# Kernel tuning notes

Hardware: AMD Instinct MI355X
Metric: run time of the kernel (lower is better)

## Reference

```python
import jax, jax.numpy as jnp
import numpy as np

NEG = -1e9  # additive mask value


def _longformer_attn(x, kv_mask, Wq, bq, Wk, bk, Wv, bv, Wqg, bqg, Wkg, bkg, Wvg, bvg, Wo, bo, H, w, G):
    # x: [B, S, E]; kv_mask: [B, S] (mask*-1 > 0 => global; first G tokens are global by construction)
    B, S, E = x.shape
    D = E // H
    scale = 1.0 / float(D) ** 0.5

    def proj(W, b):  # -> [B, H, S, D]
        return (x @ W + b).reshape(B, S, H, D).transpose(0, 2, 1, 3)

    q = proj(Wq, bq) * scale
    k = proj(Wk, bk)
    v = proj(Wv, bv)

    nc = S // w  # number of query chunks of size w
    # banded keys/values: each chunk of w queries sees a 3w key band (prev/cur/next chunk)
    idx = (jnp.arange(nc) * w)[:, None] + jnp.arange(3 * w)[None, :]  # [nc, 3w] into padded seq

    def band(t):  # [B,H,S,D] -> [B,H,nc,3w,D]
        tp = jnp.pad(t, ((0, 0), (0, 0), (w, w), (0, 0)))
        return tp[:, :, idx, :]

    k3, v3 = band(k), band(v)
    qc = q.reshape(B, H, nc, w, D)
    s_win = jnp.einsum('bhcwd,bhced->bhcwe', qc, k3)  # [B,H,nc,w,3w]

    i = jnp.arange(w)[:, None]
    j = jnp.arange(3 * w)[None, :]
    rel_ok = (j >= i) & (j <= i + 2 * w)  # |key_pos - query_pos| <= w
    keypos = (jnp.arange(nc) * w)[:, None, None] + (jnp.arange(3 * w) - w)[None, None, :]  # [nc,1,3w]
    ok = rel_ok[None] & (keypos >= 0) & (keypos < S) & (keypos >= G)  # global keys handled separately
    s_win = jnp.where(ok[None, None], s_win, NEG)

    # every query also attends to the G global keys (standard projections)
    s_g = jnp.einsum('bhqd,bhgd->bhqg', q, k[:, :, :G])  # [B,H,S,G]
    s_all = jnp.concatenate([s_g, s_win.reshape(B, H, S, 3 * w)], axis=-1)
    p = jax.nn.softmax(s_all, axis=-1)  # joint softmax over global + window keys
    p_g, p_w = p[..., :G], p[..., G:].reshape(B, H, nc, w, 3 * w)

    out = jnp.einsum('bhcwe,bhced->bhcwd', p_w, v3).reshape(B, H, S, D)
    out = out + jnp.einsum('bhqg,bhgd->bhqd', p_g, v[:, :, :G])

    # global query rows: full attention over all tokens with the *global* projections
    qg = (x @ Wqg + bqg).reshape(B, S, H, D).transpose(0, 2, 1, 3)[:, :, :G] * scale
    kg = (x @ Wkg + bkg).reshape(B, S, H, D).transpose(0, 2, 1, 3)
    vg = (x @ Wvg + bvg).reshape(B, S, H, D).transpose(0, 2, 1, 3)
    pg = jax.nn.softmax(jnp.einsum('bhgd,bhsd->bhgs', qg, kg), axis=-1)  # [B,H,G,S]
    out = out.at[:, :, :G].set(jnp.einsum('bhgs,bhsd->bhgd', pg, vg))

    ctx = out.transpose(0, 2, 1, 3).reshape(B, S, E)
    return ctx @ Wo + bo  # wrapper's self.output Linear


def setup_inputs() -> dict:
    key = jax.random.key(0)
    B, S, E, H, w, G = 2, 4096, 1024, 16, 256, 64
    ks = jax.random.split(key, 20)
    x = jax.random.normal(ks[0], (B, S, E), dtype=jnp.float32)
    # key_value_states acts as the mask source: (kv * -1) > 0 marks global tokens
    kv = jnp.zeros((B, S), dtype=jnp.float32).at[:, :G].set(-1.0)

    def lin(k1, k2):
        return (jax.random.normal(k1, (E, E), dtype=jnp.float32) * 0.02,
                jax.random.normal(k2, (E,), dtype=jnp.float32) * 0.02)

    Wq, bq = lin(ks[1], ks[2])
    Wk, bk = lin(ks[3], ks[4])
    Wv, bv = lin(ks[5], ks[6])
    Wqg, bqg = lin(ks[7], ks[8])
    Wkg, bkg = lin(ks[9], ks[10])
    Wvg, bvg = lin(ks[11], ks[12])
    Wo, bo = lin(ks[13], ks[14])
    return {"hidden_states": x, "key_value_states": kv,
            "Wq": Wq, "bq": bq, "Wk": Wk, "bk": bk, "Wv": Wv, "bv": bv,
            "Wqg": Wqg, "bqg": bqg, "Wkg": Wkg, "bkg": bkg, "Wvg": Wvg, "bvg": bvg,
            "Wo": Wo, "bo": bo, "num_heads": H, "window": w, "num_global": G}


def reference(hidden_states, key_value_states, Wq, bq, Wk, bk, Wv, bv, Wqg, bqg, Wkg, bkg, Wvg, bvg, Wo, bo, num_heads, window, num_global):
    return _longformer_attn(hidden_states, key_value_states, Wq, bq, Wk, bk, Wv, bv,
                            Wqg, bqg, Wkg, bkg, Wvg, bvg, Wo, bo,
                            num_heads, window, num_global)
```

## Files before the change

### kernel.cpp

```cpp
#include <hip/hip_runtime.h>

typedef _Float16 half_t;
typedef _Float16 h8 __attribute__((ext_vector_type(8)));
typedef _Float16 h4 __attribute__((ext_vector_type(4)));
typedef float f4 __attribute__((ext_vector_type(4)));

#define DEV __device__ __forceinline__

constexpr int Bc = 2, Sc = 4096, Ec = 1024, Hc = 16, Dc = 64, Wc = 256, Gc = 64;
constexpr float QSCALE = 0.125f;
constexpr float NEGV = -1e9f;

DEV f4 mfma16(h8 a, h8 b, f4 c) {
  return __builtin_amdgcn_mfma_f32_16x16x32_f16(a, b, c, 0, 0, 0);
}

DEV void gl_lds16(const half_t* g, half_t* l) {
  __builtin_amdgcn_global_load_lds((const __attribute__((address_space(1))) void*)g,
                                   (__attribute__((address_space(3))) void*)l, 16, 0, 0);
}


__global__ void cvt_x_kernel(const float* __restrict__ x, half_t* __restrict__ xh) {
  int i = blockIdx.x * 256 + threadIdx.x;
  float4 v = ((const float4*)x)[i];
  h4 o;
  o[0] = (half_t)v.x; o[1] = (half_t)v.y; o[2] = (half_t)v.z; o[3] = (half_t)v.w;
  ((h4*)xh)[i] = o;
}

__global__ void wcvt_kernel(const float* __restrict__ W, half_t* __restrict__ Wt) {
  __shared__ float tile[64][65];
  const int bx = blockIdx.x & 15, by = blockIdx.x >> 4;
  const int tx = threadIdx.x & 63, ty = threadIdx.x >> 6;
  const int n0 = bx * 64, k0 = by * 64;
#pragma unroll
  for (int i = 0; i < 16; ++i) {
    int k = ty + i * 4;
    tile[k][tx] = W[(size_t)(k0 + k) * Ec + n0 + tx];
  }
  __syncthreads();
#pragma unroll
  for (int i = 0; i < 16; ++i) {
    int n = ty + i * 4;
    Wt[(size_t)(n0 + n) * Ec + k0 + tx] = (half_t)tile[tx][n];
  }
}

__global__ __launch_bounds__(256) void gemm_proj(const half_t* __restrict__ A,
                                                 const half_t* __restrict__ Bt,
                                                 const float* __restrict__ bcat,
                                                 half_t* __restrict__ qh, half_t* __restrict__ kh,
                                                 half_t* __restrict__ vt, half_t* __restrict__ kgh,
                                                 half_t* __restrict__ vgt, half_t* __restrict__ qgh) {
  __shared__ __align__(16) half_t Ash[128 * 32];
  __shared__ __align__(16) half_t Bsh[128 * 32];
  const int tid = threadIdx.x;
  const int wv = tid >> 6, lane = tid & 63;
  const int mr = lane & 15, qd = lane >> 4;
  const int wv_m = wv >> 1, wv_n = wv & 1;
  const int col0 = blockIdx.x * 128;
  const int row0 = blockIdx.y * 128;
  const int g = col0 >> 10;

  f4 acc[4][4] = {};

  for (int k0 = 0; k0 < Ec; k0 += 32) {
#pragma unroll
    for (int i = 0; i < 2; ++i) {
      int slot = wv * 128 + i * 64 + lane;
      int r = slot >> 2;
      int kc = (slot & 3) ^ (r & 3);
      gl_lds16(A + (size_t)(row0 + r) * Ec + k0 + kc * 8, Ash + (size_t)(wv * 128 + i * 64) * 8);
      gl_lds16(Bt + (size_t)(col0 + r) * Ec + k0 + kc * 8, Bsh + (size_t)(wv * 128 + i * 64) * 8);
    }
    __syncthreads();
    h8 af[4], bf[4];
#pragma unroll
    for (int mt = 0; mt < 4; ++mt) {
      int r = wv_m * 64 + mt * 16 + mr;
      af[mt] = *(const h8*)(Ash + (size_t)((r << 2) | (qd ^ (r & 3))) * 8);
    }
#pragma unroll
    for (int nt = 0; nt < 4; ++nt) {
      int r = wv_n * 64 + nt * 16 + mr;
      bf[nt] = *(const h8*)(Bsh + (size_t)((r << 2) | (qd ^ (r & 3))) * 8);
    }
#pragma unroll
    for (int mt = 0; mt < 4; ++mt)
#pragma unroll
      for (int nt = 0; nt < 4; ++nt)
        acc[mt][nt] = mfma16(af[mt], bf[nt], acc[mt][nt]);
    __syncthreads();
  }

  const float scale = (g == 0 || g == 5) ? QSCALE : 1.0f;
#pragma unroll
  for (int mt = 0; mt < 4; ++mt) {
#pragma unroll
    for (int nt = 0; nt < 4; ++nt) {
      const int C = col0 + wv_n * 64 + nt * 16 + mr;
      const float bval = bcat[C];
      const int c1 = C & 1023, hh = c1 >> 6, d = c1 & 63;
      const int Rbase = row0 + wv_m * 64 + mt * 16 + qd * 4;
      f4 a = acc[mt][nt];
      if (g == 2 || g == 4) {
        half_t* O = (g == 2) ? vt : vgt;
        int b = Rbase >> 12, s = Rbase & 4095;
        h4 pk;
#pragma unroll
        for (int r = 0; r < 4; ++r) pk[r] = (half_t)(a[r] + bval);
        *(h4*)(O + ((size_t)(b * Hc + hh) * Dc + d) * Sc + s) = pk;
      } else if (g == 5) {
#pragma unroll
        for (int r = 0; r < 4; ++r) {
          int R = Rbase + r;
          int b = R >> 12, s = R & 4095;
          if (s < Gc)
            qgh[((size_t)(b * Hc + hh) * Gc + s) * Dc + d] = (half_t)((a[r] + bval) * scale);
        }
      } else {
        half_t* O = (g == 0) ? qh : (g == 1) ? kh : kgh;
#pragma unroll
        for (int r = 0; r < 4; ++r) {
          int R = Rbase + r;
          int b = R >> 12, s = R & 4095;
          O[((size_t)(b * Hc + hh) * Sc + s) * Dc + d] = (half_t)((a[r] + bval) * scale);
        }
      }
    }
  }
}

__global__ __launch_bounds__(256) void gemm_out(const half_t* __restrict__ A,
                                                const half_t* __restrict__ Bt,
                                                const float* __restrict__ bias,
                                                float* __restrict__ O) {
  __shared__ __align__(16) half_t Ash[128 * 32];
  __shared__ __align__(16) half_t Bsh[128 * 32];
  const int tid = threadIdx.x;
  const int wv = tid >> 6, lane = tid & 63;
  const int mr = lane & 15, qd = lane >> 4;
  const int wv_m = wv >> 1, wv_n = wv & 1;
  const int col0 = blockIdx.x * 128;
  const int row0 = blockIdx.y * 128;

  f4 acc[4][4] = {};

  for (int k0 = 0; k0 < Ec; k0 += 32) {
#pragma unroll
    for (int i = 0; i < 2; ++i) {
      int slot = wv * 128 + i * 64 + lane;
      int r = slot >> 2;
      int kc = (slot & 3) ^ (r & 3);
      gl_lds16(A + (size_t)(row0 + r) * Ec + k0 + kc * 8, Ash + (size_t)(wv * 128 + i * 64) * 8);
      gl_lds16(Bt + (size_t)(col0 + r) * Ec + k0 + kc * 8, Bsh + (size_t)(wv * 128 + i * 64) * 8);
    }
    __syncthreads();
    h8 af[4], bf[4];
#pragma unroll
    for (int mt = 0; mt < 4; ++mt) {
      int r = wv_m * 64 + mt * 16 + mr;
      af[mt] = *(const h8*)(Ash + (size_t)((r << 2) | (qd ^ (r & 3))) * 8);
    }
#pragma unroll
    for (int nt = 0; nt < 4; ++nt) {
      int r = wv_n * 64 + nt * 16 + mr;
      bf[nt] = *(const h8*)(Bsh + (size_t)((r << 2) | (qd ^ (r & 3))) * 8);
    }
#pragma unroll
    for (int mt = 0; mt < 4; ++mt)
#pragma unroll
      for (int nt = 0; nt < 4; ++nt)
        acc[mt][nt] = mfma16(af[mt], bf[nt], acc[mt][nt]);
    __syncthreads();
  }

#pragma unroll
  for (int mt = 0; mt < 4; ++mt) {
#pragma unroll
    for (int nt = 0; nt < 4; ++nt) {
      const int C = col0 + wv_n * 64 + nt * 16 + mr;
      const float bval = bias[C];
      const int Rbase = row0 + wv_m * 64 + mt * 16 + qd * 4;
      f4 a = acc[mt][nt];
#pragma unroll
      for (int r = 0; r < 4; ++r)
        O[(size_t)(Rbase + r) * Ec + C] = a[r] + bval;
    }
  }
}

__global__ __launch_bounds__(256) void win_attn(const half_t* __restrict__ qh,
                                                const half_t* __restrict__ kh,
                                                const half_t* __restrict__ vt,
                                                half_t* __restrict__ ctx) {
  constexpr int PST = 88;
  __shared__ __align__(16) half_t Kb[2][64 * 64];
  __shared__ __align__(16) half_t Vb[2][64 * 64];
  __shared__ __align__(16) half_t Pl[4][16 * PST];
  const int bid = blockIdx.x;
  const int qc = bid & 15, h = (bid >> 4) & 15, b = bid >> 8;
  const int qs = qc << 8;
  const int tid = threadIdx.x, wv = tid >> 6, lane = tid & 63;
  const int mr = lane & 15, qd = lane >> 4;
  const int qw = qs + wv * 64;
  const size_t bh = (size_t)(b * Hc + h);
  const half_t* qb = qh + bh * Sc * Dc;
  const half_t* kb = kh + bh * Sc * Dc;
  const half_t* vb = vt + bh * Dc * Sc;
  half_t* Pw = &Pl[wv][0];

  h8 qf[4][2];
#pragma unroll
  for (int qt = 0; qt < 4; ++qt) {
    const half_t* qrow = qb + (size_t)(qw + qt * 16 + mr) * Dc;
    qf[qt][0] = *(const h8*)(qrow + qd * 8);
    qf[qt][1] = *(const h8*)(qrow + 32 + qd * 8);
  }

  int tiles[14];
  int nT = 0;
  tiles[nT++] = 0;
  {
    int lo = qs - Wc; if (lo < Gc) lo = Gc;
    int hi = qs + 448; if (hi > Sc - 64) hi = Sc - 64;
    for (int kp0 = lo; kp0 <= hi; kp0 += 64) tiles[nT++] = kp0;
  }

  auto stage = [&](int kp0, int bi) {
#pragma unroll
    for (int i = 0; i < 2; ++i) {
      const int seg = wv * 2 + i;
      const int s = seg * 64 + lane;
      const int r = s >> 3;
      const int kc = (s & 7) ^ (r & 7);
      gl_lds16(kb + (size_t)(kp0 + r) * Dc + kc * 8, &Kb[bi][seg * 512]);
      gl_lds16(vb + (size_t)r * Sc + kp0 + kc * 8, &Vb[bi][seg * 512]);
    }
  };

  float m_run[4], l_run[4];
  f4 acc[4][4] = {};
#pragma unroll
  for (int qt = 0; qt < 4; ++qt) { m_run[qt] = -1e30f; l_run[qt] = 0.f; }

  stage(tiles[0], 0);

  for (int t = 0; t < nT; ++t) {
    __syncthreads();
    if (t + 1 < nT) stage(tiles[t + 1], (t + 1) & 1);
    const int kp0 = tiles[t];
    if (t > 0 && (kp0 > qw + 319 || kp0 + 63 < qw - Wc)) continue;

    const half_t* BK = Kb[t & 1];
    const half_t* BV = Vb[t & 1];
    h8 kf[4][2], vf[4][2];
#pragma unroll
    for (int mt = 0; mt < 4; ++mt) {
      const int row = mt * 16 + mr, r7 = row & 7;
      kf[mt][0] = *(const h8*)(BK + (size_t)(row * 8 + (qd ^ r7)) * 8);
      kf[mt][1] = *(const h8*)(BK + (size_t)(row * 8 + ((qd + 4) ^ r7)) * 8);
      vf[mt][0] = *(const h8*)(BV + (size_t)(row * 8 + (qd ^ r7)) * 8);
      vf[mt][1] = *(const h8*)(BV + (size_t)(row * 8 + ((qd + 4) ^ r7)) * 8);
    }
    const bool nomask = (t == 0) || (kp0 >= qw - 193 && kp0 <= qw + 193);

#pragma unroll
    for (int qt = 0; qt < 4; ++qt) {
      f4 sa[4];
#pragma unroll
      for (int mt = 0; mt < 4; ++mt) {
        f4 s = {};
        s = mfma16(kf[mt][0], qf[qt][0], s);
        s = mfma16(kf[mt][1], qf[qt][1], s);
        sa[mt] = s;
      }
      const int q = qw + qt * 16 + mr;
      if (!nomask) {
#pragma unroll
        for (int mt = 0; mt < 4; ++mt)
#pragma unroll
          for (int r = 0; r < 4; ++r) {
            const int kp = kp0 + mt * 16 + qd * 4 + r;
            if (kp < q - Wc || kp > q + Wc) sa[mt][r] = NEGV;
          }
      }
      float tm = -1e30f;
#pragma unroll
      for (int mt = 0; mt < 4; ++mt)
#pragma unroll
        for (int r = 0; r < 4; ++r) tm = fmaxf(tm, sa[mt][r]);
      tm = fmaxf(tm, __shfl_xor(tm, 16));
      tm = fmaxf(tm, __shfl_xor(tm, 32));
      const float mnew = fmaxf(m_run[qt], tm);
      const float alpha = __expf(m_run[qt] - mnew);
      m_run[qt] = mnew;
      float psum = 0.0f;
#pragma unroll
      for (int mt = 0; mt < 4; ++mt) {
        h4 pk;
#pragma unroll
        for (int r = 0; r < 4; ++r) {
          const float p = __expf(sa[mt][r] - mnew);
          psum += p;
          pk[r] = (half_t)p;
        }
        *(h4*)(Pw + mr * PST + mt * 16 + qd * 4) = pk;
      }
      psum += __shfl_xor(psum, 16);
      psum += __shfl_xor(psum, 32);
      l_run[qt] = l_run[qt] * alpha + psum;
#pragma unroll
      for (int mt = 0; mt < 4; ++mt)
#pragma unroll
        for (int r = 0; r < 4; ++r) acc[qt][mt][r] *= alpha;
      const h8 p0 = *(const h8*)(Pw + mr * PST + qd * 8);
      const h8 p1 = *(const h8*)(Pw + mr * PST + 32 + qd * 8);
#pragma unroll
      for (int mt = 0; mt < 4; ++mt) {
        acc[qt][mt] = mfma16(vf[mt][0], p0, acc[qt][mt]);
        acc[qt][mt] = mfma16(vf[mt][1], p1, acc[qt][mt]);
      }
    }
  }

#pragma unroll
  for (int qt = 0; qt < 4; ++qt) {
    const float inv = 1.0f / l_run[qt];
    const int q = qw + qt * 16 + mr;
    half_t* crow = ctx + ((size_t)(b * Sc) + q) * Ec + h * Dc;
#pragma unroll
    for (int mt = 0; mt < 4; ++mt) {
      h4 pk;
#pragma unroll
      for (int r = 0; r < 4; ++r) pk[r] = (half_t)(acc[qt][mt][r] * inv);
      *(h4*)(crow + mt * 16 + qd * 4) = pk;
    }
  }
}


__global__ __launch_bounds__(256) void gq_scores(const half_t* __restrict__ qgh,
                                                 const half_t* __restrict__ kgh,
                                                 float* __restrict__ Sg) {
  const int st = blockIdx.x & 15, h = (blockIdx.x >> 4) & 15, b = blockIdx.x >> 8;
  const int wv = threadIdx.x >> 6, lane = threadIdx.x & 63;
  const int mr = lane & 15, qd = lane >> 4;
  const size_t bh = (size_t)(b * Hc + h);
  const half_t* qb = qgh + bh * Gc * Dc;
  const half_t* kb = kgh + bh * Sc * Dc;
  float* out = Sg + bh * Gc * Sc;

  h8 a0 = *(const h8*)(qb + (size_t)(wv * 16 + mr) * Dc + qd * 8);
  h8 a1 = *(const h8*)(qb + (size_t)(wv * 16 + mr) * Dc + 32 + qd * 8);
#pragma unroll 4
  for (int nt = 0; nt < 16; ++nt) {
    int s = st * 256 + nt * 16 + mr;
    h8 b0 = *(const h8*)(kb + (size_t)s * Dc + qd * 8);
    h8 b1 = *(const h8*)(kb + (size_t)s * Dc + 32 + qd * 8);
    f4 scv = {};
    scv = mfma16(a0, b0, scv);
    scv = mfma16(a1, b1, scv);
#pragma unroll
    for (int r = 0; r < 4; ++r)
      out[(size_t)(wv * 16 + qd * 4 + r) * Sc + st * 256 + nt * 16 + mr] = scv[r];
  }
}

__global__ __launch_bounds__(256) void gq_softmax(const float* __restrict__ Sg,
                                                  half_t* __restrict__ Pg) {
  const int row = blockIdx.x;
  const float* src = Sg + (size_t)row * Sc;
  half_t* dst = Pg + (size_t)row * Sc;
  const int t = threadIdx.x;
  __shared__ float red[4], reds[4];
  float mx = -1e30f;
  for (int i = t; i < Sc; i += 256) mx = fmaxf(mx, src[i]);
#pragma unroll
  for (int o = 1; o < 64; o <<= 1) mx = fmaxf(mx, __shfl_xor(mx, o));
  if ((t & 63) == 0) red[t >> 6] = mx;
  __syncthreads();
  mx = fmaxf(fmaxf(red[0], red[1]), fmaxf(red[2], red[3]));
  float pv[16];
  float sum = 0.f;
  for (int i = t, j = 0; i < Sc; i += 256, ++j) {
    pv[j] = __expf(src[i] - mx);
    sum += pv[j];
  }
#pragma unroll
  for (int o = 1; o < 64; o <<= 1) sum += __shfl_xor(sum, o);
  if ((t & 63) == 0) reds[t >> 6] = sum;
  __syncthreads();
  sum = reds[0] + reds[1] + reds[2] + reds[3];
  float inv = 1.0f / sum;
  for (int i = t, j = 0; i < Sc; i += 256, ++j) dst[i] = (half_t)(pv[j] * inv);
}

__global__ __launch_bounds__(256) void gq_pv(const half_t* __restrict__ Pg,
                                             const half_t* __restrict__ vgt,
                                             half_t* __restrict__ ctx) {
  const int ds = blockIdx.x & 3, h = (blockIdx.x >> 2) & 15, b = blockIdx.x >> 6;
  const int wv = threadIdx.x >> 6, lane = threadIdx.x & 63;
  const int mr = lane & 15, qd = lane >> 4;
  const size_t bh = (size_t)(b * Hc + h);
  const half_t* pb = Pg + bh * Gc * Sc;
  const int d = ds * 16 + mr;
  const half_t* vb = vgt + (bh * Dc + d) * Sc;
  f4 o = {};
  for (int ch = 0; ch < 128; ++ch) {
    h8 af = *(const h8*)(pb + (size_t)(wv * 16 + mr) * Sc + ch * 32 + qd * 8);
    h8 bf = *(const h8*)(vb + ch * 32 + qd * 8);
    o = mfma16(af, bf, o);
  }
#pragma unroll
  for (int r = 0; r < 4; ++r) {
    int g = wv * 16 + qd * 4 + r;
    ctx[(size_t)(b * Sc + g) * Ec + h * Dc + d] = (half_t)o[r];
  }
}


extern "C" void kernel_launch(void* const* d_in, const int* in_sizes, int n_in,
                              void* d_out, int out_size, void* d_ws, size_t ws_size,
                              hipStream_t stream) {
  const float* x   = (const float*)d_in[0];
  const float* Wq  = (const float*)d_in[2];
  const float* bq  = (const float*)d_in[3];
  const float* Wk  = (const float*)d_in[4];
  const float* bk  = (const float*)d_in[5];
  const float* Wv  = (const float*)d_in[6];
  const float* bv  = (const float*)d_in[7];
  const float* Wqg = (const float*)d_in[8];
  const float* bqg = (const float*)d_in[9];
  const float* Wkg = (const float*)d_in[10];
  const float* bkg = (const float*)d_in[11];
  const float* Wvg = (const float*)d_in[12];
  const float* bvg = (const float*)d_in[13];
  const float* Wo  = (const float*)d_in[14];
  const float* bo  = (const float*)d_in[15];
  float* out = (float*)d_out;

  char* ws = (char*)d_ws;
  size_t off = 0;
  auto alloc = [&](size_t bytes) {
    void* p = ws + off;
    off = (off + bytes + 255) & ~(size_t)255;
    return p;
  };
  const size_t BSE2 = (size_t)Bc * Sc * Ec * 2;
  const size_t W2 = (size_t)Ec * Ec * 2;
  half_t* xh   = (half_t*)alloc(BSE2);
  half_t* Wcat = (half_t*)alloc(W2 * 6);
  half_t* WtO  = (half_t*)alloc(W2);
  float*  bcat = (float*)alloc(6 * Ec * 4);
  half_t* qh   = (half_t*)alloc(BSE2);
  half_t* kh   = (half_t*)alloc(BSE2);
  half_t* vt   = (half_t*)alloc(BSE2);
  half_t* kgh  = (half_t*)alloc(BSE2);
  half_t* vgt  = (half_t*)alloc(BSE2);
  half_t* qgh  = (half_t*)alloc((size_t)Bc * Hc * Gc * Dc * 2);
  half_t* ctx  = (half_t*)alloc(BSE2);
  float*  Sg   = (float*)alloc((size_t)Bc * Hc * Gc * Sc * 4);
  half_t* Pg   = (half_t*)alloc((size_t)Bc * Hc * Gc * Sc * 2);
  (void)ws_size; (void)in_sizes; (void)n_in; (void)out_size;

  cvt_x_kernel<<<8192, 256, 0, stream>>>(x, xh);
  wcvt_kernel<<<256, 256, 0, stream>>>(Wq,  Wcat + 0 * Ec * Ec);
  wcvt_kernel<<<256, 256, 0, stream>>>(Wk,  Wcat + 1 * (size_t)Ec * Ec);
  wcvt_kernel<<<256, 256, 0, stream>>>(Wv,  Wcat + 2 * (size_t)Ec * Ec);
  wcvt_kernel<<<256, 256, 0, stream>>>(Wkg, Wcat + 3 * (size_t)Ec * Ec);
  wcvt_kernel<<<256, 256, 0, stream>>>(Wvg, Wcat + 4 * (size_t)Ec * Ec);
  wcvt_kernel<<<256, 256, 0, stream>>>(Wqg, Wcat + 5 * (size_t)Ec * Ec);
  wcvt_kernel<<<256, 256, 0, stream>>>(Wo,  WtO);
  hipMemcpyAsync(bcat + 0 * Ec, bq,  Ec * 4, hipMemcpyDeviceToDevice, stream);
  hipMemcpyAsync(bcat + 1 * Ec, bk,  Ec * 4, hipMemcpyDeviceToDevice, stream);
  hipMemcpyAsync(bcat + 2 * Ec, bv,  Ec * 4, hipMemcpyDeviceToDevice, stream);
  hipMemcpyAsync(bcat + 3 * Ec, bkg, Ec * 4, hipMemcpyDeviceToDevice, stream);
  hipMemcpyAsync(bcat + 4 * Ec, bvg, Ec * 4, hipMemcpyDeviceToDevice, stream);
  hipMemcpyAsync(bcat + 5 * Ec, bqg, Ec * 4, hipMemcpyDeviceToDevice, stream);

  gemm_proj<<<dim3(48, 64), 256, 0, stream>>>(xh, Wcat, bcat, qh, kh, vt, kgh, vgt, qgh);

  win_attn<<<Bc * Hc * (Sc / 256), 256, 0, stream>>>(qh, kh, vt, ctx);

  gq_scores<<<Bc * Hc * 16, 256, 0, stream>>>(qgh, kgh, Sg);
  gq_softmax<<<Bc * Hc * Gc, 256, 0, stream>>>(Sg, Pg);
  gq_pv<<<Bc * Hc * 4, 256, 0, stream>>>(Pg, vgt, ctx);

  gemm_out<<<dim3(8, 64), 256, 0, stream>>>(ctx, WtO, bo, out);
}
```

Baseline: 486.1 us.

## Compute global-query projection only for global rows and batch weight conversions

The global-query projection is split out of the big projection GEMM into a small dedicated GEMM that computes only the 64 global rows per batch, instead of the full sequence whose other rows were thrown away. The seven weight-conversion launches become one 2D-grid kernel, and the six bias memcpys are dropped by passing the bias pointers straight into the GEMM. The LDS swizzle is changed to XOR with (r>>1)&3 to alter the bank-conflict pattern. In exchange there is one extra small launch with only 8 blocks, and the swizzle change could help or hurt LDS conflicts.

```diff
diff --git a/kernel.cpp b/kernel.cpp
--- a/kernel.cpp
+++ b/kernel.cpp
@@ -29,8 +29,17 @@
   ((h4*)xh)[i] = o;
 }
 
-__global__ void wcvt_kernel(const float* __restrict__ W, half_t* __restrict__ Wt) {
+__global__ void wcvt_all(const float* __restrict__ Wq, const float* __restrict__ Wk,
+                         const float* __restrict__ Wv, const float* __restrict__ Wkg,
+                         const float* __restrict__ Wvg, const float* __restrict__ Wqg,
+                         const float* __restrict__ Wo,
+                         half_t* __restrict__ Wcat, half_t* __restrict__ WtQg,
+                         half_t* __restrict__ WtO) {
   __shared__ float tile[64][65];
+  const int y = blockIdx.y;
+  const float* W = (y == 0) ? Wq : (y == 1) ? Wk : (y == 2) ? Wv :
+                   (y == 3) ? Wkg : (y == 4) ? Wvg : (y == 5) ? Wqg : Wo;
+  half_t* Wt = (y < 5) ? (Wcat + (size_t)y * Ec * Ec) : (y == 5) ? WtQg : WtO;
   const int bx = blockIdx.x & 15, by = blockIdx.x >> 4;
   const int tx = threadIdx.x & 63, ty = threadIdx.x >> 6;
   const int n0 = bx * 64, k0 = by * 64;
@@ -49,10 +58,14 @@
 
 __global__ __launch_bounds__(256) void gemm_proj(const half_t* __restrict__ A,
                                                  const half_t* __restrict__ Bt,
-                                                 const float* __restrict__ bcat,
+                                                 const float* __restrict__ bq,
+                                                 const float* __restrict__ bk,
+                                                 const float* __restrict__ bv,
+                                                 const float* __restrict__ bkg,
+                                                 const float* __restrict__ bvg,
                                                  half_t* __restrict__ qh, half_t* __restrict__ kh,
                                                  half_t* __restrict__ vt, half_t* __restrict__ kgh,
-                                                 half_t* __restrict__ vgt, half_t* __restrict__ qgh) {
+                                                 half_t* __restrict__ vgt) {
   __shared__ __align__(16) half_t Ash[128 * 32];
   __shared__ __align__(16) half_t Bsh[128 * 32];
   const int tid = threadIdx.x;
@@ -62,6 +75,7 @@
   const int col0 = blockIdx.x * 128;
   const int row0 = blockIdx.y * 128;
   const int g = col0 >> 10;
+  const float* bptr = (g == 0) ? bq : (g == 1) ? bk : (g == 2) ? bv : (g == 3) ? bkg : bvg;
 
   f4 acc[4][4] = {};
 
@@ -70,7 +84,7 @@
     for (int i = 0; i < 2; ++i) {
       int slot = wv * 128 + i * 64 + lane;
       int r = slot >> 2;
-      int kc = (slot & 3) ^ (r & 3);
+      int kc = (slot & 3) ^ ((r >> 1) & 3);
       gl_lds16(A + (size_t)(row0 + r) * Ec + k0 + kc * 8, Ash + (size_t)(wv * 128 + i * 64) * 8);
       gl_lds16(Bt + (size_t)(col0 + r) * Ec + k0 + kc * 8, Bsh + (size_t)(wv * 128 + i * 64) * 8);
     }
@@ -79,12 +93,12 @@
 #pragma unroll
     for (int mt = 0; mt < 4; ++mt) {
       int r = wv_m * 64 + mt * 16 + mr;
-      af[mt] = *(const h8*)(Ash + (size_t)((r << 2) | (qd ^ (r & 3))) * 8);
+      af[mt] = *(const h8*)(Ash + (size_t)((r << 2) | (qd ^ ((r >> 1) & 3))) * 8);
     }
 #pragma unroll
     for (int nt = 0; nt < 4; ++nt) {
       int r = wv_n * 64 + nt * 16 + mr;
-      bf[nt] = *(const h8*)(Bsh + (size_t)((r << 2) | (qd ^ (r & 3))) * 8);
+      bf[nt] = *(const h8*)(Bsh + (size_t)((r << 2) | (qd ^ ((r >> 1) & 3))) * 8);
     }
 #pragma unroll
     for (int mt = 0; mt < 4; ++mt)
@@ -94,14 +108,14 @@
     __syncthreads();
   }
 
-  const float scale = (g == 0 || g == 5) ? QSCALE : 1.0f;
+  const float scale = (g == 0) ? QSCALE : 1.0f;
 #pragma unroll
   for (int mt = 0; mt < 4; ++mt) {
 #pragma unroll
     for (int nt = 0; nt < 4; ++nt) {
       const int C = col0 + wv_n * 64 + nt * 16 + mr;
-      const float bval = bcat[C];
       const int c1 = C & 1023, hh = c1 >> 6, d = c1 & 63;
+      const float bval = bptr[c1];
       const int Rbase = row0 + wv_m * 64 + mt * 16 + qd * 4;
       f4 a = acc[mt][nt];
       if (g == 2 || g == 4) {
@@ -111,14 +125,6 @@
 #pragma unroll
         for (int r = 0; r < 4; ++r) pk[r] = (half_t)(a[r] + bval);
         *(h4*)(O + ((size_t)(b * Hc + hh) * Dc + d) * Sc + s) = pk;
-      } else if (g == 5) {
-#pragma unroll
-        for (int r = 0; r < 4; ++r) {
-          int R = Rbase + r;
-          int b = R >> 12, s = R & 4095;
-          if (s < Gc)
-            qgh[((size_t)(b * Hc + hh) * Gc + s) * Dc + d] = (half_t)((a[r] + bval) * scale);
-        }
       } else {
         half_t* O = (g == 0) ? qh : (g == 1) ? kh : kgh;
 #pragma unroll
@@ -127,6 +133,69 @@
           int b = R >> 12, s = R & 4095;
           O[((size_t)(b * Hc + hh) * Sc + s) * Dc + d] = (half_t)((a[r] + bval) * scale);
         }
+      }
+    }
+  }
+}
+
+__global__ __launch_bounds__(256) void gemm_qg(const half_t* __restrict__ A,
+                                               const half_t* __restrict__ Bt,
+                                               const float* __restrict__ bqg,
+                                               half_t* __restrict__ qgh) {
+  __shared__ __align__(16) half_t Ash[128 * 32];
+  __shared__ __align__(16) half_t Bsh[128 * 32];
+  const int tid = threadIdx.x;
+  const int wv = tid >> 6, lane = tid & 63;
+  const int mr = lane & 15, qd = lane >> 4;
+  const int wv_m = wv >> 1, wv_n = wv & 1;
+  const int col0 = blockIdx.x * 128;
+
+  f4 acc[4][4] = {};
+
+  for (int k0 = 0; k0 < Ec; k0 += 32) {
+#pragma unroll
+    for (int i = 0; i < 2; ++i) {
+      int slot = wv * 128 + i * 64 + lane;
+      int r = slot >> 2;
+      int grow = (r < 64) ? r : (4032 + r);
+      int kc = (slot & 3) ^ ((r >> 1) & 3);
+      gl_lds16(A + (size_t)grow * Ec + k0 + kc * 8, Ash + (size_t)(wv * 128 + i * 64) * 8);
+      gl_lds16(Bt + (size_t)(col0 + r) * Ec + k0 + kc * 8, Bsh + (size_t)(wv * 128 + i * 64) * 8);
+    }
+    __syncthreads();
+    h8 af[4], bf[4];
+#pragma unroll
+    for (int mt = 0; mt < 4; ++mt) {
+      int r = wv_m * 64 + mt * 16 + mr;
+      af[mt] = *(const h8*)(Ash + (size_t)((r << 2) | (qd ^ ((r >> 1) & 3))) * 8);
+    }
+#pragma unroll
+    for (int nt = 0; nt < 4; ++nt) {
+      int r = wv_n * 64 + nt * 16 + mr;
+      bf[nt] = *(const h8*)(Bsh + (size_t)((r << 2) | (qd ^ ((r >> 1) & 3))) * 8);
+    }
+#pragma unroll
+    for (int mt = 0; mt < 4; ++mt)
+#pragma unroll
+      for (int nt = 0; nt < 4; ++nt)
+        acc[mt][nt] = mfma16(af[mt], bf[nt], acc[mt][nt]);
+    __syncthreads();
+  }
+
+#pragma unroll
+  for (int mt = 0; mt < 4; ++mt) {
+#pragma unroll
+    for (int nt = 0; nt < 4; ++nt) {
+      const int C = col0 + wv_n * 64 + nt * 16 + mr;
+      const int hh = C >> 6, d = C & 63;
+      const float bval = bqg[C];
+      const int Rbase = wv_m * 64 + mt * 16 + qd * 4;
+      f4 a = acc[mt][nt];
+#pragma unroll
+      for (int r = 0; r < 4; ++r) {
+        int rr = Rbase + r;
+        int b = rr >> 6, s = rr & 63;
+        qgh[((size_t)(b * Hc + hh) * Gc + s) * Dc + d] = (half_t)((a[r] + bval) * QSCALE);
       }
     }
   }
@@ -152,7 +221,7 @@
     for (int i = 0; i < 2; ++i) {
       int slot = wv * 128 + i * 64 + lane;
       int r = slot >> 2;
-      int kc = (slot & 3) ^ (r & 3);
+      int kc = (slot & 3) ^ ((r >> 1) & 3);
       gl_lds16(A + (size_t)(row0 + r) * Ec + k0 + kc * 8, Ash + (size_t)(wv * 128 + i * 64) * 8);
       gl_lds16(Bt + (size_t)(col0 + r) * Ec + k0 + kc * 8, Bsh + (size_t)(wv * 128 + i * 64) * 8);
     }
@@ -161,12 +230,12 @@
 #pragma unroll
     for (int mt = 0; mt < 4; ++mt) {
       int r = wv_m * 64 + mt * 16 + mr;
-      af[mt] = *(const h8*)(Ash + (size_t)((r << 2) | (qd ^ (r & 3))) * 8);
+      af[mt] = *(const h8*)(Ash + (size_t)((r << 2) | (qd ^ ((r >> 1) & 3))) * 8);
     }
 #pragma unroll
     for (int nt = 0; nt < 4; ++nt) {
       int r = wv_n * 64 + nt * 16 + mr;
-      bf[nt] = *(const h8*)(Bsh + (size_t)((r << 2) | (qd ^ (r & 3))) * 8);
+      bf[nt] = *(const h8*)(Bsh + (size_t)((r << 2) | (qd ^ ((r >> 1) & 3))) * 8);
     }
 #pragma unroll
     for (int mt = 0; mt < 4; ++mt)
@@ -451,9 +520,9 @@
   const size_t BSE2 = (size_t)Bc * Sc * Ec * 2;
   const size_t W2 = (size_t)Ec * Ec * 2;
   half_t* xh   = (half_t*)alloc(BSE2);
-  half_t* Wcat = (half_t*)alloc(W2 * 6);
+  half_t* Wcat = (half_t*)alloc(W2 * 5);
+  half_t* WtQg = (half_t*)alloc(W2);
   half_t* WtO  = (half_t*)alloc(W2);
-  float*  bcat = (float*)alloc(6 * Ec * 4);
   half_t* qh   = (half_t*)alloc(BSE2);
   half_t* kh   = (half_t*)alloc(BSE2);
   half_t* vt   = (half_t*)alloc(BSE2);
@@ -466,21 +535,11 @@
   (void)ws_size; (void)in_sizes; (void)n_in; (void)out_size;
 
   cvt_x_kernel<<<8192, 256, 0, stream>>>(x, xh);
-  wcvt_kernel<<<256, 256, 0, stream>>>(Wq,  Wcat + 0 * Ec * Ec);
-  wcvt_kernel<<<256, 256, 0, stream>>>(Wk,  Wcat + 1 * (size_t)Ec * Ec);
-  wcvt_kernel<<<256, 256, 0, stream>>>(Wv,  Wcat + 2 * (size_t)Ec * Ec);
-  wcvt_kernel<<<256, 256, 0, stream>>>(Wkg, Wcat + 3 * (size_t)Ec * Ec);
-  wcvt_kernel<<<256, 256, 0, stream>>>(Wvg, Wcat + 4 * (size_t)Ec * Ec);
-  wcvt_kernel<<<256, 256, 0, stream>>>(Wqg, Wcat + 5 * (size_t)Ec * Ec);
-  wcvt_kernel<<<256, 256, 0, stream>>>(Wo,  WtO);
-  hipMemcpyAsync(bcat + 0 * Ec, bq,  Ec * 4, hipMemcpyDeviceToDevice, stream);
-  hipMemcpyAsync(bcat + 1 * Ec, bk,  Ec * 4, hipMemcpyDeviceToDevice, stream);
-  hipMemcpyAsync(bcat + 2 * Ec, bv,  Ec * 4, hipMemcpyDeviceToDevice, stream);
-  hipMemcpyAsync(bcat + 3 * Ec, bkg, Ec * 4, hipMemcpyDeviceToDevice, stream);
-  hipMemcpyAsync(bcat + 4 * Ec, bvg, Ec * 4, hipMemcpyDeviceToDevice, stream);
-  hipMemcpyAsync(bcat + 5 * Ec, bqg, Ec * 4, hipMemcpyDeviceToDevice, stream);
-
-  gemm_proj<<<dim3(48, 64), 256, 0, stream>>>(xh, Wcat, bcat, qh, kh, vt, kgh, vgt, qgh);
+  wcvt_all<<<dim3(256, 7), 256, 0, stream>>>(Wq, Wk, Wv, Wkg, Wvg, Wqg, Wo, Wcat, WtQg, WtO);
+
+  gemm_proj<<<dim3(40, 64), 256, 0, stream>>>(xh, Wcat, bq, bk, bv, bkg, bvg,
+                                              qh, kh, vt, kgh, vgt);
+  gemm_qg<<<8, 256, 0, stream>>>(xh, WtQg, bqg, qgh);
 
   win_attn<<<Bc * Hc * (Sc / 256), 256, 0, stream>>>(qh, kh, vt, ctx);
 
```

Measured after the change: 458.7 us. 5.6% less time.
